# Optimization experiments

Hardware: AMD Instinct MI355X
Metric: run time of the kernel (lower is better)

The kernel has to match this reference:

```python
import jax, jax.numpy as jnp
import numpy as np

GROUPS = 8
EPS = 1e-5


def group_norm(x, gamma, beta):
    # x: (b, c, h, w); normalize per sample over each group of c//GROUPS channels and all spatial dims
    b, c, h, w = x.shape
    xg = x.reshape(b, GROUPS, c // GROUPS, h, w)
    mean = jnp.mean(xg, axis=(2, 3, 4), keepdims=True)
    var = jnp.var(xg, axis=(2, 3, 4), keepdims=True)
    xn = ((xg - mean) * jax.lax.rsqrt(var + EPS)).reshape(b, c, h, w)
    return xn * gamma[None, :, None, None] + beta[None, :, None, None]


def setup_inputs() -> dict:
    key = jax.random.key(0)
    k1, k2, k3 = jax.random.split(key, 3)
    b, c, h, w = 32, 256, 32, 32
    x = jax.random.normal(k1, (b, c, h, w), dtype=jnp.float32)
    qkv_w = jax.random.normal(k2, (3 * c, c), dtype=jnp.float32) * 0.02
    qkv_b = jnp.zeros((3 * c,), dtype=jnp.float32)
    out_w = jax.random.normal(k3, (c, c), dtype=jnp.float32) * 0.02
    out_b = jnp.zeros((c,), dtype=jnp.float32)
    gn_gamma = jnp.ones((c,), dtype=jnp.float32)
    gn_beta = jnp.zeros((c,), dtype=jnp.float32)
    return {"x": x, "gn_gamma": gn_gamma, "gn_beta": gn_beta,
            "qkv_w": qkv_w, "qkv_b": qkv_b, "out_w": out_w, "out_b": out_b}


def reference(x, gn_gamma, gn_beta, qkv_w, qkv_b, out_w, out_b):
    b, c, h, w = x.shape
    xn = group_norm(x, gn_gamma, gn_beta)
    # 1x1 conv == per-pixel linear: (b,c,h,w) x (3c,c) -> (b,3c,h,w)
    qkv = jnp.einsum('bchw,dc->bdhw', xn, qkv_w) + qkv_b[None, :, None, None]
    q, k, v = jnp.split(qkv, 3, axis=1)
    # (b, c, h, w) -> (b, hw, c)
    def tok(t):
        return t.transpose(0, 2, 3, 1).reshape(b, h * w, c)
    q, k, v = tok(q), tok(k), tok(v)
    scale = 1.0 / jnp.sqrt(jnp.asarray(c, dtype=x.dtype))
    scores = jnp.einsum('bnc,bmc->bnm', q, k) * scale  # (b, hw, hw)
    attn = jax.nn.softmax(scores, axis=-1)
    out = jnp.einsum('bnm,bmc->bnc', attn, v)  # (b, hw, c)
    out = out.reshape(b, h, w, c).transpose(0, 3, 1, 2)  # (b, c, h, w)
    out = jnp.einsum('bchw,dc->bdhw', out, out_w) + out_b[None, :, None, None]
    return out + x
```

## Files before the change

### kernel.cpp

```cpp
#include <hip/hip_runtime.h>
#include <hip/hip_bf16.h>
#include <stdint.h>


typedef __bf16 bf16_t;
typedef __bf16 bf16x4 __attribute__((ext_vector_type(4)));
typedef __bf16 bf16x8 __attribute__((ext_vector_type(8)));
typedef float f32x16 __attribute__((ext_vector_type(16)));
typedef _Float16 f16x4 __attribute__((ext_vector_type(4)));

#define MFMA32(a, b, c) __builtin_amdgcn_mfma_f32_32x32x16_bf16((a), (b), (c), 0, 0, 0)
#define GLL16(g, l)                                                                      \
    __builtin_amdgcn_global_load_lds((const __attribute__((address_space(1))) void*)(g), \
                                     (__attribute__((address_space(3))) void*)(l), 16, 0, 0)
#define WAITV0 asm volatile("s_waitcnt vmcnt(0)" ::: "memory")
#define SBAR   __builtin_amdgcn_s_barrier()

#define QSCALE 0.0901684400555f

__global__ __launch_bounds__(512) void gn_kernel(const float* __restrict__ x,
                                                 const float* __restrict__ gamma,
                                                 const float* __restrict__ beta,
                                                 bf16_t* __restrict__ xn,
                                                 const float* __restrict__ s1,
                                                 bf16_t* __restrict__ d1, int n1,
                                                 const float* __restrict__ s2,
                                                 bf16_t* __restrict__ d2, int n2) {
    if (blockIdx.x >= 256) {
        int i = (blockIdx.x - 256) * 512 + threadIdx.x;
        int stride = 32 * 512;
        for (int k = i; k < n1; k += stride) d1[k] = (bf16_t)s1[k];
        for (int k = i; k < n2; k += stride) d2[k] = (bf16_t)s2[k];
        return;
    }
    extern __shared__ char gsm[];
    float* red = (float*)(gsm + 65536);
    int bg = blockIdx.x, b = bg >> 3, g = bg & 7;
    const float* base = x + (size_t)(b * 256 + g * 32) * 1024;
    int tid = threadIdx.x;
    int half = tid >> 8, col = tid & 255;

    float s = 0.f, ss = 0.f;
    #pragma unroll 4
    for (int c2 = 0; c2 < 16; c2++) {
        int c = c2 * 2 + half;
        float4 v = *(const float4*)(base + c * 1024 + col * 4);
        s += v.x + v.y + v.z + v.w;
        ss += v.x * v.x + v.y * v.y + v.z * v.z + v.w * v.w;
        f16x4 h = {(_Float16)v.x, (_Float16)v.y, (_Float16)v.z, (_Float16)v.w};
        *(f16x4*)(gsm + c * 2048 + ((col * 8) ^ ((c & 7) << 4))) = h;
    }
    for (int off = 32; off; off >>= 1) { s += __shfl_down(s, off); ss += __shfl_down(ss, off); }
    if ((tid & 63) == 0) { red[tid >> 6] = s; red[8 + (tid >> 6)] = ss; }
    __syncthreads();
    float S = 0.f, SS = 0.f;
    #pragma unroll
    for (int k = 0; k < 8; k++) { S += red[k]; SS += red[8 + k]; }
    float mean = S * (1.0f / 32768.0f);
    float var = SS * (1.0f / 32768.0f) - mean * mean;
    float rstd = rsqrtf(var + 1e-5f);

    int c = tid & 31;
    float gam = gamma[g * 32 + c] * rstd;
    float bet = beta[g * 32 + c] - mean * gam;
    bf16_t* dst = xn + (size_t)(b * 1024) * 256 + g * 32 + c;
    #pragma unroll 4
    for (int it = 0; it < 64; it++) {
        int p = it * 16 + (tid >> 5);
        _Float16 hv = *(_Float16*)(gsm + c * 2048 + ((p * 2) ^ ((c & 7) << 4)));
        dst[(size_t)p * 256] = (bf16_t)((float)hv * gam + bet);
    }
}

__global__ __launch_bounds__(512, 2) void gemm_qkv(const bf16_t* __restrict__ xn,
                                                   const bf16_t* __restrict__ wq,
                                                   const float* __restrict__ qkv_b,
                                                   bf16_t* __restrict__ qb,
                                                   bf16_t* __restrict__ kb,
                                                   bf16_t* __restrict__ vt) {
    extern __shared__ char smem[];
    char* As = smem;
    int tid = threadIdx.x, wv = tid >> 6, lane = tid & 63;
    int l31 = lane & 31, hi = lane >> 5;
    int t0 = blockIdx.x * 128;
    const char* asrc = (const char*)xn + (size_t)t0 * 512;
    const char* wsrc = (const char*)wq;

    {
        int u = lane & 31, rofs = lane >> 5;
        #pragma unroll
        for (int t = 0; t < 8; t++) {
            int r0 = wv * 16 + t * 2;
            int r = r0 + rofs;
            GLL16(asrc + (size_t)r * 512 + ((u ^ (r & 31)) * 16), As + r0 * 512);
        }
    }
    auto stage_B = [&](int nt) {
        char* Bd = smem + 65536 + (nt & 1) * 32768;
        int u = lane & 31, rofs = lane >> 5;
        #pragma unroll
        for (int t = 0; t < 4; t++) {
            int r0 = wv * 8 + t * 2;
            int r = r0 + rofs;
            GLL16(wsrc + (size_t)(nt * 64 + r) * 512 + ((u ^ (r & 31)) * 16), Bd + r0 * 512);
        }
    };
    stage_B(0);
    WAITV0; SBAR;

    int wm = wv >> 1, wd = wv & 1;
    int bb = t0 >> 10, pos0 = t0 & 1023;

    for (int nt = 0; nt < 12; nt++) {
        if (nt < 11) stage_B(nt + 1);
        const char* Bs = smem + 65536 + (nt & 1) * 32768;
        f32x16 acc = {};
        if (nt < 8) {
            __builtin_amdgcn_s_setprio(1);
            #pragma unroll
            for (int ks = 0; ks < 16; ks++) {
                int col = ks * 32 + hi * 16;
                bf16x8 a = *(const bf16x8*)(As + (wm * 32 + l31) * 512 + (col ^ (l31 << 4)));
                bf16x8 bfr = *(const bf16x8*)(Bs + (wd * 32 + l31) * 512 + (col ^ (l31 << 4)));
                acc = MFMA32(a, bfr, acc);
            }
            __builtin_amdgcn_s_setprio(0);
            int d = nt * 64 + wd * 32 + l31;
            bool isq = nt < 4;
            float bias = qkv_b[d];
            bf16_t* dst = isq ? qb : kb;
            int dd = isq ? d : d - 256;
            float sc = isq ? QSCALE : 1.0f;
            #pragma unroll
            for (int r = 0; r < 16; r++) {
                int tok = t0 + wm * 32 + (r & 3) + 8 * (r >> 2) + 4 * hi;
                dst[(size_t)tok * 256 + dd] = (bf16_t)((acc[r] + bias) * sc);
            }
        } else {
            __builtin_amdgcn_s_setprio(1);
            #pragma unroll
            for (int ks = 0; ks < 16; ks++) {
                int col = ks * 32 + hi * 16;
                bf16x8 a = *(const bf16x8*)(As + (wm * 32 + l31) * 512 + (col ^ (l31 << 4)));
                bf16x8 bfr = *(const bf16x8*)(Bs + (wd * 32 + l31) * 512 + (col ^ (l31 << 4)));
                acc = MFMA32(bfr, a, acc);
            }
            __builtin_amdgcn_s_setprio(0);
            int dbase = (nt - 8) * 64 + wd * 32;
            int pos = pos0 + wm * 32 + l31;
            #pragma unroll
            for (int r = 0; r < 16; r++) {
                int d = dbase + (r & 3) + 8 * (r >> 2) + 4 * hi;
                vt[(size_t)bb * 262144 + (size_t)d * 1024 + pos] =
                    (bf16_t)(acc[r] + qkv_b[512 + d]);
            }
        }
        if (nt < 11) { WAITV0; SBAR; }
    }
}

__global__ __launch_bounds__(256, 1) void attn_kernel(const bf16_t* __restrict__ qb,
                                                      const bf16_t* __restrict__ kb,
                                                      const bf16_t* __restrict__ vt,
                                                      bf16_t* __restrict__ ao) {
    extern __shared__ char smem[];
    int tid = threadIdx.x, i = blockIdx.x;
    int b = (i & 7) + ((i >> 6) << 3);
    int qt = (i >> 3) & 7;
    int wv = tid >> 6, lane = tid & 63, l31 = lane & 31, hi = lane >> 5;

    const char* kbase = (const char*)kb + (size_t)b * 524288;
    const char* vbase = (const char*)vt + (size_t)b * 524288;
    char* Pw = smem + 131072 + wv * 4096;

    int qg = qt * 128 + wv * 32 + l31;
    const char* qsrc = (const char*)qb + (size_t)(b * 1024 + qg) * 512;
    bf16x8 qf[16];
    #pragma unroll
    for (int ks = 0; ks < 16; ks++) qf[ks] = *(const bf16x8*)(qsrc + ks * 32 + hi * 16);

    f32x16 o[8] = {};
    float mrun = -1e30f, lrun = 0.f;

    auto stage = [&](int ch) {
        char* Kd = smem + (ch & 1) * 32768;
        char* Vd = smem + 65536 + (ch & 1) * 32768;
        int j0 = ch * 64;
        #pragma unroll
        for (int t = 0; t < 8; t++) {
            int r0 = wv * 16 + t * 2;
            int r = r0 + (lane >> 5), u = lane & 31;
            GLL16(kbase + (size_t)(j0 + r) * 512 + ((u ^ (r & 31)) * 16), Kd + r0 * 512);
        }
        #pragma unroll
        for (int h = 0; h < 2; h++) {
            #pragma unroll
            for (int p = 0; p < 4; p++) {
                int Ls = (tid << 4) + (p << 12);
                int s = Ls ^ (((Ls >> 7) & 3) << 4);
                GLL16(vbase + (size_t)(s >> 6) * 2048 + j0 * 2 + h * 64 + (s & 63),
                      Vd + h * 16384 + (p << 12) + wv * 1024);
            }
        }
    };

    stage(0);
    __syncthreads();

    for (int ch = 0; ch < 16; ch++) {
        const char* Ks = smem + (ch & 1) * 32768;
        const char* Vs = smem + 65536 + (ch & 1) * 32768;
        if (ch < 15) stage(ch + 1);

        f32x16 sv0 = {}, sv1 = {};
        #pragma unroll
        for (int ks = 0; ks < 16; ks++) {
            int col = ks * 32 + hi * 16;
            bf16x8 k0 = *(const bf16x8*)(Ks + l31 * 512 + (col ^ (l31 << 4)));
            bf16x8 k1 = *(const bf16x8*)(Ks + (32 + l31) * 512 + (col ^ (l31 << 4)));
            sv0 = MFMA32(k0, qf[ks], sv0);
            sv1 = MFMA32(k1, qf[ks], sv1);
        }

        float mc = -1e30f;
        #pragma unroll
        for (int r = 0; r < 16; r++) mc = fmaxf(mc, fmaxf(sv0[r], sv1[r]));
        mc = fmaxf(mc, __shfl_xor(mc, 32));
        float mo = mrun;
        float mn = (mc <= mo + 8.0f) ? mo : mc;
        float rs = 0.f;
        #pragma unroll
        for (int r = 0; r < 16; r++) {
            sv0[r] = exp2f(sv0[r] - mn);
            sv1[r] = exp2f(sv1[r] - mn);
            rs += sv0[r] + sv1[r];
        }
        rs += __shfl_xor(rs, 32);
        float al = exp2f(mo - mn);
        lrun = lrun * al + rs;
        mrun = mn;

        #pragma unroll
        for (int rg = 0; rg < 4; rg++) {
            bf16x4 pa, pb;
            #pragma unroll
            for (int r = 0; r < 4; r++) {
                pa[r] = (bf16_t)sv0[rg * 4 + r];
                pb[r] = (bf16_t)sv1[rg * 4 + r];
            }
            int sw = (l31 & 7) << 4;
            *(bf16x4*)(Pw + l31 * 128 + ((rg * 16 + hi * 8) ^ sw)) = pa;
            *(bf16x4*)(Pw + l31 * 128 + ((64 + rg * 16 + hi * 8) ^ sw)) = pb;
        }
        if (__any(mn != mo)) {
            #pragma unroll
            for (int dt = 0; dt < 8; dt++) o[dt] = o[dt] * al;
        }

        #pragma unroll
        for (int pk = 0; pk < 4; pk++) {
            int pcol = (pk * 32 + hi * 16) ^ ((l31 & 7) << 4);
            bf16x8 pf = *(const bf16x8*)(Pw + l31 * 128 + pcol);
            const char* Vh = Vs + (pk >> 1) * 16384;
            #pragma unroll
            for (int dt = 0; dt < 8; dt++) {
                int d = dt * 32 + l31;
                int a = (d * 64 + (pk & 1) * 32 + hi * 16) ^ (((d >> 1) & 3) << 4);
                bf16x8 vf = *(const bf16x8*)(Vh + a);
                o[dt] = MFMA32(vf, pf, o[dt]);
            }
        }
        __syncthreads();
    }

    float inv = 1.0f / lrun;
    char* aod = (char*)ao + (size_t)(b * 1024 + qg) * 512;
    #pragma unroll
    for (int dt = 0; dt < 8; dt++) {
        #pragma unroll
        for (int rg = 0; rg < 4; rg++) {
            bf16x4 w;
            #pragma unroll
            for (int r = 0; r < 4; r++) w[r] = (bf16_t)(o[dt][rg * 4 + r] * inv);
            *(bf16x4*)(aod + dt * 64 + rg * 16 + hi * 8) = w;
        }
    }
}

__global__ __launch_bounds__(512, 2) void gemm_out(const bf16_t* __restrict__ wo,
                                                   const bf16_t* __restrict__ ao,
                                                   const float* __restrict__ out_b,
                                                   const float* __restrict__ x,
                                                   float* __restrict__ out) {
    extern __shared__ char smem[];
    char* Bs = smem;
    int tid = threadIdx.x, wv = tid >> 6, lane = tid & 63;
    int l31 = lane & 31, hi = lane >> 5;
    int t0 = blockIdx.x * 128;
    const char* bsrc = (const char*)ao + (size_t)t0 * 512;
    const char* wsrc = (const char*)wo;

    {
        int u = lane & 31, rofs = lane >> 5;
        #pragma unroll
        for (int t = 0; t < 8; t++) {
            int r0 = wv * 16 + t * 2;
            int r = r0 + rofs;
            GLL16(bsrc + (size_t)r * 512 + ((u ^ (r & 31)) * 16), Bs + r0 * 512);
        }
    }
    auto stage_W = [&](int ct) {
        char* Wd = smem + 65536 + (ct & 1) * 32768;
        int u = lane & 31, rofs = lane >> 5;
        #pragma unroll
        for (int t = 0; t < 4; t++) {
            int r0 = wv * 8 + t * 2;
            int r = r0 + rofs;
            GLL16(wsrc + (size_t)(ct * 64 + r) * 512 + ((u ^ (r & 31)) * 16), Wd + r0 * 512);
        }
    };
    stage_W(0);
    WAITV0; SBAR;

    int wm = wv >> 1, wc = wv & 1;
    int bb = t0 >> 10, pos0 = t0 & 1023;

    for (int ct = 0; ct < 4; ct++) {
        if (ct < 3) stage_W(ct + 1);
        const char* Ws = smem + 65536 + (ct & 1) * 32768;
        f32x16 acc = {};
        __builtin_amdgcn_s_setprio(1);
        #pragma unroll
        for (int ks = 0; ks < 16; ks++) {
            int col = ks * 32 + hi * 16;
            bf16x8 w = *(const bf16x8*)(Ws + (wc * 32 + l31) * 512 + (col ^ (l31 << 4)));
            bf16x8 bf = *(const bf16x8*)(Bs + (wm * 32 + l31) * 512 + (col ^ (l31 << 4)));
            acc = MFMA32(w, bf, acc);
        }
        __builtin_amdgcn_s_setprio(0);
        int pos = pos0 + wm * 32 + l31;
        #pragma unroll
        for (int r = 0; r < 16; r++) {
            int c = ct * 64 + wc * 32 + (r & 3) + 8 * (r >> 2) + 4 * hi;
            size_t idx = ((size_t)bb * 256 + c) * 1024 + pos;
            out[idx] = acc[r] + out_b[c] + x[idx];
        }
        if (ct < 3) { WAITV0; SBAR; }
    }
}

extern "C" void kernel_launch(void* const* d_in, const int* in_sizes, int n_in,
                              void* d_out, int out_size, void* d_ws, size_t ws_size,
                              hipStream_t stream) {
    (void)in_sizes; (void)n_in; (void)out_size; (void)ws_size;
    const float* x      = (const float*)d_in[0];
    const float* gamma  = (const float*)d_in[1];
    const float* beta   = (const float*)d_in[2];
    const float* qkv_w  = (const float*)d_in[3];
    const float* qkv_b  = (const float*)d_in[4];
    const float* out_w  = (const float*)d_in[5];
    const float* out_b  = (const float*)d_in[6];
    float* out = (float*)d_out;

    char* ws = (char*)d_ws;
    const size_t MB16 = 16777216;
    bf16_t* xn  = (bf16_t*)(ws);
    bf16_t* qb  = (bf16_t*)(ws + 1 * MB16);
    bf16_t* kb  = (bf16_t*)(ws + 2 * MB16);
    bf16_t* vt  = (bf16_t*)(ws + 3 * MB16);
    bf16_t* ao  = (bf16_t*)(ws + 4 * MB16);
    bf16_t* wqb = (bf16_t*)(ws + 5 * MB16);
    bf16_t* wob = (bf16_t*)(ws + 5 * MB16 + 393216);

    gn_kernel<<<288, 512, 65600, stream>>>(x, gamma, beta, xn,
                                           qkv_w, wqb, 196608, out_w, wob, 65536);
    gemm_qkv<<<256, 512, 131072, stream>>>(xn, wqb, qkv_b, qb, kb, vt);
    attn_kernel<<<256, 256, 147456, stream>>>(qb, kb, vt, ao);
    gemm_out<<<256, 512, 131072, stream>>>(wob, ao, out_b, x, out);
}
```

Measured before the change: 121.5 us.

## Shrink attention blocks to two waves with single-buffered 32-key chunks

The attention kernel now uses 128-thread blocks covering 64 queries, launched as 512 blocks, with 32-key K/V chunks held in a single LDS buffer of about 36 KB instead of a double-buffered 147 KB layout. This lets several blocks fit per CU and more work spread across CUs. In exchange it drops the prefetch overlap: each chunk is loaded and waited on with barriers before compute. K and V are also re-fetched twice as often per query across blocks.

```diff
diff --git a/kernel.cpp b/kernel.cpp
--- a/kernel.cpp
+++ b/kernel.cpp
@@ -159,21 +159,21 @@
     }
 }
 
-__global__ __launch_bounds__(256, 1) void attn_kernel(const bf16_t* __restrict__ qb,
+__global__ __launch_bounds__(128, 2) void attn_kernel(const bf16_t* __restrict__ qb,
                                                       const bf16_t* __restrict__ kb,
                                                       const bf16_t* __restrict__ vt,
                                                       bf16_t* __restrict__ ao) {
     extern __shared__ char smem[];
     int tid = threadIdx.x, i = blockIdx.x;
-    int b = (i & 7) + ((i >> 6) << 3);
-    int qt = (i >> 3) & 7;
+    int b = (i & 7) + ((i >> 7) << 3);
+    int qt = (i >> 3) & 15;
     int wv = tid >> 6, lane = tid & 63, l31 = lane & 31, hi = lane >> 5;
 
     const char* kbase = (const char*)kb + (size_t)b * 524288;
     const char* vbase = (const char*)vt + (size_t)b * 524288;
-    char* Pw = smem + 131072 + wv * 4096;
-
-    int qg = qt * 128 + wv * 32 + l31;
+    char* Pw = smem + 32768 + wv * 2048;
+
+    int qg = qt * 64 + wv * 32 + l31;
     const char* qsrc = (const char*)qb + (size_t)(b * 1024 + qg) * 512;
     bf16x8 qf[16];
     #pragma unroll
@@ -183,57 +183,49 @@
     float mrun = -1e30f, lrun = 0.f;
 
     auto stage = [&](int ch) {
-        char* Kd = smem + (ch & 1) * 32768;
-        char* Vd = smem + 65536 + (ch & 1) * 32768;
-        int j0 = ch * 64;
+        int j0 = ch * 32;
         #pragma unroll
         for (int t = 0; t < 8; t++) {
-            int r0 = wv * 16 + t * 2;
-            int r = r0 + (lane >> 5), u = lane & 31;
-            GLL16(kbase + (size_t)(j0 + r) * 512 + ((u ^ (r & 31)) * 16), Kd + r0 * 512);
-        }
-        #pragma unroll
-        for (int h = 0; h < 2; h++) {
-            #pragma unroll
-            for (int p = 0; p < 4; p++) {
-                int Ls = (tid << 4) + (p << 12);
-                int s = Ls ^ (((Ls >> 7) & 3) << 4);
-                GLL16(vbase + (size_t)(s >> 6) * 2048 + j0 * 2 + h * 64 + (s & 63),
-                      Vd + h * 16384 + (p << 12) + wv * 1024);
-            }
+            int Ls = tid * 16 + t * 2048;
+            int r = Ls >> 9, u = (Ls >> 4) & 31;
+            GLL16(kbase + (size_t)(j0 + r) * 512 + ((u ^ r) << 4),
+                  smem + wv * 1024 + t * 2048);
+        }
+        #pragma unroll
+        for (int t = 0; t < 8; t++) {
+            int Ls = tid * 16 + t * 2048;
+            int s = Ls ^ (((Ls >> 7) & 3) << 4);
+            GLL16(vbase + (size_t)(s >> 6) * 2048 + ch * 64 + (s & 63),
+                  smem + 16384 + wv * 1024 + t * 2048);
         }
     };
 
     stage(0);
-    __syncthreads();
-
-    for (int ch = 0; ch < 16; ch++) {
-        const char* Ks = smem + (ch & 1) * 32768;
-        const char* Vs = smem + 65536 + (ch & 1) * 32768;
-        if (ch < 15) stage(ch + 1);
-
-        f32x16 sv0 = {}, sv1 = {};
+    WAITV0; SBAR;
+
+    const char* Ks = smem;
+    const char* Vs = smem + 16384;
+
+    for (int ch = 0; ch < 32; ch++) {
+        f32x16 sv = {};
         #pragma unroll
         for (int ks = 0; ks < 16; ks++) {
             int col = ks * 32 + hi * 16;
             bf16x8 k0 = *(const bf16x8*)(Ks + l31 * 512 + (col ^ (l31 << 4)));
-            bf16x8 k1 = *(const bf16x8*)(Ks + (32 + l31) * 512 + (col ^ (l31 << 4)));
-            sv0 = MFMA32(k0, qf[ks], sv0);
-            sv1 = MFMA32(k1, qf[ks], sv1);
+            sv = MFMA32(k0, qf[ks], sv);
         }
 
         float mc = -1e30f;
         #pragma unroll
-        for (int r = 0; r < 16; r++) mc = fmaxf(mc, fmaxf(sv0[r], sv1[r]));
+        for (int r = 0; r < 16; r++) mc = fmaxf(mc, sv[r]);
         mc = fmaxf(mc, __shfl_xor(mc, 32));
         float mo = mrun;
         float mn = (mc <= mo + 8.0f) ? mo : mc;
         float rs = 0.f;
         #pragma unroll
         for (int r = 0; r < 16; r++) {
-            sv0[r] = exp2f(sv0[r] - mn);
-            sv1[r] = exp2f(sv1[r] - mn);
-            rs += sv0[r] + sv1[r];
+            sv[r] = exp2f(sv[r] - mn);
+            rs += sv[r];
         }
         rs += __shfl_xor(rs, 32);
         float al = exp2f(mo - mn);
@@ -242,15 +234,10 @@
 
         #pragma unroll
         for (int rg = 0; rg < 4; rg++) {
-            bf16x4 pa, pb;
-            #pragma unroll
-            for (int r = 0; r < 4; r++) {
-                pa[r] = (bf16_t)sv0[rg * 4 + r];
-                pb[r] = (bf16_t)sv1[rg * 4 + r];
-            }
-            int sw = (l31 & 7) << 4;
-            *(bf16x4*)(Pw + l31 * 128 + ((rg * 16 + hi * 8) ^ sw)) = pa;
-            *(bf16x4*)(Pw + l31 * 128 + ((64 + rg * 16 + hi * 8) ^ sw)) = pb;
+            bf16x4 pa;
+            #pragma unroll
+            for (int r = 0; r < 4; r++) pa[r] = (bf16_t)sv[rg * 4 + r];
+            *(bf16x4*)(Pw + l31 * 64 + rg * 16 + hi * 8) = pa;
         }
         if (__any(mn != mo)) {
             #pragma unroll
@@ -258,19 +245,22 @@
         }
 
         #pragma unroll
-        for (int pk = 0; pk < 4; pk++) {
-            int pcol = (pk * 32 + hi * 16) ^ ((l31 & 7) << 4);
-            bf16x8 pf = *(const bf16x8*)(Pw + l31 * 128 + pcol);
-            const char* Vh = Vs + (pk >> 1) * 16384;
+        for (int pk = 0; pk < 2; pk++) {
+            bf16x8 pf = *(const bf16x8*)(Pw + l31 * 64 + pk * 32 + hi * 16);
             #pragma unroll
             for (int dt = 0; dt < 8; dt++) {
                 int d = dt * 32 + l31;
-                int a = (d * 64 + (pk & 1) * 32 + hi * 16) ^ (((d >> 1) & 3) << 4);
-                bf16x8 vf = *(const bf16x8*)(Vh + a);
+                int a = (d * 64 + pk * 32 + hi * 16) ^ (((d >> 1) & 3) << 4);
+                bf16x8 vf = *(const bf16x8*)(Vs + a);
                 o[dt] = MFMA32(vf, pf, o[dt]);
             }
         }
-        __syncthreads();
+
+        SBAR;
+        if (ch < 31) {
+            stage(ch + 1);
+            WAITV0; SBAR;
+        }
     }
 
     float inv = 1.0f / lrun;
@@ -375,6 +365,6 @@
     gn_kernel<<<288, 512, 65600, stream>>>(x, gamma, beta, xn,
                                            qkv_w, wqb, 196608, out_w, wob, 65536);
     gemm_qkv<<<256, 512, 131072, stream>>>(xn, wqb, qkv_b, qb, kb, vt);
-    attn_kernel<<<256, 256, 147456, stream>>>(qb, kb, vt, ao);
+    attn_kernel<<<512, 128, 36864, stream>>>(qb, kb, vt, ao);
     gemm_out<<<256, 512, 131072, stream>>>(wob, ao, out_b, x, out);
 }
```

Measured after the change: 180.3 us. 48.4% more time.
